# Kernel tuning notes

Measured on AMD Instinct MI355X. Metric: run time of the kernel, lower is better.

## Reference

```python
import jax, jax.numpy as jnp
import numpy as np

H = 16          # num_attention_heads
HD = 64         # attention_head_size
D = H * HD
SCALE = HD ** -0.5
SP_HEADS = np.array([0, 2, 4, 6, 8, 10, 12, 14])   # sparsemax heads
SM_HEADS = np.array([1, 3, 5, 7, 9, 11, 13, 15])   # softmax heads


def sparsemax(z):
    # z: [..., K]; sparsemax along last dim (Martins & Astudillo 2016)
    K = z.shape[-1]
    zs = -jnp.sort(-z, axis=-1)                      # descending sort
    k = jnp.arange(1, K + 1, dtype=z.dtype)
    cs = jnp.cumsum(zs, axis=-1)
    support = (1 + k * zs) > cs
    ksel = jnp.sum(support, axis=-1, keepdims=True)  # support size >= 1
    tau = (jnp.take_along_axis(cs, ksel - 1, axis=-1) - 1) / ksel.astype(z.dtype)
    return jnp.maximum(z - tau, 0)


def setup_inputs() -> dict:
    key = jax.random.key(0)
    ks = jax.random.split(key, 4)
    B, S = 4, 1024
    return {
        "hidden_states": jax.random.normal(ks[0], (B, S, D), dtype=jnp.float32),
        "Wq": jax.random.normal(ks[1], (D, D), dtype=jnp.float32) * 0.02,
        "bq": jnp.zeros((D,), dtype=jnp.float32),
        "Wk": jax.random.normal(ks[2], (D, D), dtype=jnp.float32) * 0.02,
        "bk": jnp.zeros((D,), dtype=jnp.float32),
        "Wv": jax.random.normal(ks[3], (D, D), dtype=jnp.float32) * 0.02,
        "bv": jnp.zeros((D,), dtype=jnp.float32),
        "attention_mask": jnp.zeros((B, 1, 1, S), dtype=jnp.float32),
    }


def reference(hidden_states, Wq, bq, Wk, bk, Wv, bv, attention_mask):
    B, S, _ = hidden_states.shape

    def proj(W, b):
        # [B,S,D] -> [B,H,S,HD]
        return (hidden_states @ W + b).reshape(B, S, H, HD).transpose(0, 2, 1, 3)

    q, k, v = proj(Wq, bq), proj(Wk, bk), proj(Wv, bv)
    scores = jnp.einsum('bhqd,bhkd->bhqk', q, k) * SCALE
    scores = scores + attention_mask
    scores = jnp.maximum(scores, -10000.0)           # clamp(min=-10000)
    weights = jnp.zeros_like(scores)
    weights = weights.at[:, SP_HEADS].set(sparsemax(scores[:, SP_HEADS]))
    weights = weights.at[:, SM_HEADS].set(jax.nn.softmax(scores[:, SM_HEADS], axis=-1))
    # dropout_p = 0 in eval mode
    attn_out = jnp.einsum('bhqk,bhkd->bhqd', weights, v)
    attn_out = attn_out.transpose(0, 2, 1, 3).reshape(B, S, D)
    return attn_out
```

## Files before the change

### kernel.cpp

```cpp
#include <hip/hip_runtime.h>
#include <hip/hip_bf16.h>
#include <stdint.h>

#define NH 16
#define HD 64
#define DM 1024
#define NB 4
#define SEQ 1024
#define NTOK (NB*SEQ)
#define SCALE 0.125f

typedef __bf16 bf16_t;
typedef __bf16 bf16x8 __attribute__((ext_vector_type(8)));
typedef __bf16 bf16x4 __attribute__((ext_vector_type(4)));
typedef float f32x4 __attribute__((ext_vector_type(4)));

typedef __attribute__((address_space(3))) unsigned char lds_byte;
typedef __attribute__((address_space(1))) const unsigned char gbl_byte;

__device__ __forceinline__ void glds16(const void* g, void* l){
  __builtin_amdgcn_global_load_lds((gbl_byte*)g, (lds_byte*)l, 16, 0, 0);
}

__global__ void cvt_hs_kernel(const float* __restrict__ in, bf16_t* __restrict__ out, int n4){
  int i = blockIdx.x*256 + threadIdx.x;
  if (i >= n4) return;
  f32x4 v = ((const f32x4*)in)[i];
  bf16x4 o;
  o[0]=(bf16_t)v[0]; o[1]=(bf16_t)v[1]; o[2]=(bf16_t)v[2]; o[3]=(bf16_t)v[3];
  ((bf16x4*)out)[i] = o;
}

__global__ void cvt_wt_kernel(const float* __restrict__ Wq, const float* __restrict__ Wk,
                              const float* __restrict__ Wv, bf16_t* __restrict__ outbase){
  __shared__ float tile[32][33];
  const float* W = blockIdx.z==0 ? Wq : (blockIdx.z==1 ? Wk : Wv);
  bf16_t* Wt = outbase + (size_t)blockIdx.z * DM * DM;
  int k0 = blockIdx.x*32, n0 = blockIdx.y*32;
  #pragma unroll
  for (int i=0;i<4;i++){
    int r = threadIdx.y + i*8;
    tile[r][threadIdx.x] = W[(size_t)(k0+r)*DM + n0 + threadIdx.x];
  }
  __syncthreads();
  #pragma unroll
  for (int i=0;i<4;i++){
    int r = threadIdx.y + i*8;
    Wt[(size_t)(n0+r)*DM + k0 + threadIdx.x] = (bf16_t)tile[threadIdx.x][r];
  }
}

__global__ __launch_bounds__(256)
void qkv_gemm_kernel(const bf16_t* __restrict__ Ag, const bf16_t* __restrict__ Wtb,
                     const float* __restrict__ bq, const float* __restrict__ bk, const float* __restrict__ bv,
                     bf16_t* __restrict__ Qb, bf16_t* __restrict__ Kb, bf16_t* __restrict__ Vtb)
{
  __shared__ __align__(16) bf16_t Asm[128*64];
  __shared__ __align__(16) bf16_t Bsm[128*64];
  const int z = blockIdx.z;
  const bf16_t* Btg = Wtb + (size_t)z*DM*DM;
  const float* bias = (z==0)?bq:((z==1)?bk:bv);
  const int m0 = blockIdx.x*128, n0 = blockIdx.y*128;
  const int tid = threadIdx.x, lane = tid&63, w = tid>>6;
  const int wr = w>>1, wc = w&1;
  const int lr = lane&15, hk = (lane>>4)<<3;

  f32x4 acc[4][4];
  #pragma unroll
  for (int a=0;a<4;a++)
    #pragma unroll
    for (int c=0;c<4;c++)
      acc[a][c] = (f32x4){0.f,0.f,0.f,0.f};

  for (int k0=0; k0<DM; k0+=64){
    #pragma unroll
    for (int i=0;i<4;i++){
      int cb = (i<<8) + (tid & 448);
      int flat = cb + lane;
      int row = flat>>3, kc = (flat&7)<<3;
      glds16(&Ag [(size_t)(m0+row)*DM + k0 + kc], &Asm[cb<<3]);
      glds16(&Btg[(size_t)(n0+row)*DM + k0 + kc], &Bsm[cb<<3]);
    }
    __syncthreads();
    #pragma unroll
    for (int kk=0;kk<2;kk++){
      bf16x8 af[4], bfv[4];
      #pragma unroll
      for (int mf=0;mf<4;mf++)
        af[mf] = *(const bf16x8*)&Asm[((wr*64 + mf*16 + lr)<<6) + (kk<<5) + hk];
      #pragma unroll
      for (int nf=0;nf<4;nf++)
        bfv[nf] = *(const bf16x8*)&Bsm[((wc*64 + nf*16 + lr)<<6) + (kk<<5) + hk];
      #pragma unroll
      for (int mf=0;mf<4;mf++)
        #pragma unroll
        for (int nf=0;nf<4;nf++)
          acc[mf][nf] = __builtin_amdgcn_mfma_f32_16x16x32_bf16(af[mf], bfv[nf], acc[mf][nf], 0, 0, 0);
    }
    __syncthreads();
  }

  const int q4 = (lane>>4)<<2;
  #pragma unroll
  for (int mf=0;mf<4;mf++){
    #pragma unroll
    for (int nf=0;nf<4;nf++){
      int gn = n0 + wc*64 + nf*16 + lr;
      float bsv = bias[gn];
      int hh = gn>>6, hd = gn&63;
      int gm0 = m0 + wr*64 + mf*16 + q4;
      int bb = gm0>>10, sq0 = gm0&1023;
      if (z < 2){
        bf16_t* dst = (z==0)?Qb:Kb;
        #pragma unroll
        for (int j=0;j<4;j++)
          dst[(((size_t)bb*NH + hh)*SEQ + (sq0+j))*HD + hd] = (bf16_t)(acc[mf][nf][j] + bsv);
      } else {
        bf16x4 pk;
        #pragma unroll
        for (int j=0;j<4;j++) pk[j] = (bf16_t)(acc[mf][nf][j] + bsv);
        *(bf16x4*)&Vtb[(((size_t)bb*NH + hh)*HD + hd)*SEQ + sq0] = pk;
      }
    }
  }
}

__device__ __forceinline__ void red4sum(float v[4]){
  #pragma unroll
  for (int m=32;m>=1;m>>=1){
    float t0=__shfl_xor(v[0],m,64), t1=__shfl_xor(v[1],m,64);
    float t2=__shfl_xor(v[2],m,64), t3=__shfl_xor(v[3],m,64);
    v[0]+=t0; v[1]+=t1; v[2]+=t2; v[3]+=t3;
  }
}
__device__ __forceinline__ void red4max(float v[4]){
  #pragma unroll
  for (int m=32;m>=1;m>>=1){
    float t0=__shfl_xor(v[0],m,64), t1=__shfl_xor(v[1],m,64);
    float t2=__shfl_xor(v[2],m,64), t3=__shfl_xor(v[3],m,64);
    v[0]=fmaxf(v[0],t0); v[1]=fmaxf(v[1],t1); v[2]=fmaxf(v[2],t2); v[3]=fmaxf(v[3],t3);
  }
}

__global__ __launch_bounds__(512, 4)
void attn_mfma2_kernel(const bf16_t* __restrict__ Qg, const bf16_t* __restrict__ Kg,
                       const bf16_t* __restrict__ Vt, const float* __restrict__ maskg,
                       float* __restrict__ outg)
{
  __shared__ __align__(16) bf16_t Sb[32*1024];
  char* Sbb = (char*)Sb;

  const int bh = blockIdx.y, b = bh>>4, h = bh&15;
  const int row0 = blockIdx.x*32;
  const int tid = threadIdx.x, lane = tid&63, w = tid>>6;
  const int ln = lane&15, hi4 = lane>>4;
  const size_t hoff = (size_t)bh*SEQ*HD;
  const int kbase = w*128;

  bf16x8 qf[2][2];
  #pragma unroll
  for (int mt=0; mt<2; ++mt)
    #pragma unroll
    for (int kt=0; kt<2; ++kt)
      qf[mt][kt] = *(const bf16x8*)&Qg[hoff + (size_t)(row0 + mt*16 + ln)*HD + kt*32 + hi4*8];

  #pragma unroll
  for (int nt=0; nt<8; ++nt){
    const int krow = kbase + nt*16;
    bf16x8 kf0 = *(const bf16x8*)&Kg[hoff + (size_t)(krow+ln)*HD +  0 + hi4*8];
    bf16x8 kf1 = *(const bf16x8*)&Kg[hoff + (size_t)(krow+ln)*HD + 32 + hi4*8];
    f32x4 mv = *(const f32x4*)&maskg[(size_t)b*SEQ + krow + hi4*4];
    #pragma unroll
    for (int mt=0; mt<2; ++mt){
      f32x4 acc = (f32x4){0.f,0.f,0.f,0.f};
      acc = __builtin_amdgcn_mfma_f32_16x16x32_bf16(kf0, qf[mt][0], acc, 0,0,0);
      acc = __builtin_amdgcn_mfma_f32_16x16x32_bf16(kf1, qf[mt][1], acc, 0,0,0);
      bf16x4 pk;
      #pragma unroll
      for (int j=0;j<4;++j)
        pk[j] = (bf16_t)fmaxf(fmaf(acc[j], SCALE, mv[j]), -10000.f);
      const int q = mt*16 + ln;
      const int g = (krow + hi4*4) >> 3;
      const int gp = g ^ ln;
      *(bf16x4*)(Sbb + q*2048 + gp*16 + (hi4&1)*8) = pk;
    }
  }
  __syncthreads();

  float z[4][16];
  const int qr = w*4;
  #pragma unroll
  for (int r=0;r<4;++r){
    const int q = qr + r;
    #pragma unroll
    for (int i=0;i<4;++i){
      const int gp = (i*32 + (lane>>1)) ^ (q&15);
      bf16x4 v4 = *(const bf16x4*)(Sbb + q*2048 + gp*16 + (lane&1)*8);
      z[r][i*4+0]=(float)v4[0]; z[r][i*4+1]=(float)v4[1];
      z[r][i*4+2]=(float)v4[2]; z[r][i*4+3]=(float)v4[3];
    }
  }
  __syncthreads();

  float mx[4];
  #pragma unroll
  for (int r=0;r<4;++r){
    float m = z[r][0];
    #pragma unroll
    for (int i=1;i<16;++i) m = fmaxf(m, z[r][i]);
    mx[r] = m;
  }
  red4max(mx);

  if ((h&1)==0){
    float lo[4], hi_[4];
    #pragma unroll
    for (int r=0;r<4;++r){ lo[r]=mx[r]-1.0f; hi_[r]=mx[r]; }
    for (int it=0; it<8; ++it){
      float mid[4], g4[4];
      #pragma unroll
      for (int r=0;r<4;++r){
        mid[r] = 0.5f*(lo[r]+hi_[r]);
        float g = 0.f;
        #pragma unroll
        for (int i=0;i<16;++i) g += fmaxf(z[r][i]-mid[r], 0.f);
        g4[r] = g;
      }
      red4sum(g4);
      #pragma unroll
      for (int r=0;r<4;++r){
        if (g4[r] >= 1.0f) lo[r] = mid[r]; else hi_[r] = mid[r];
      }
    }
    float tau[4];
    #pragma unroll
    for (int r=0;r<4;++r) tau[r] = lo[r];
    for (int it=0; it<3; ++it){
      float cnt[4], sm[4];
      #pragma unroll
      for (int r=0;r<4;++r){
        float c=0.f, s=0.f;
        #pragma unroll
        for (int i=0;i<16;++i){
          bool in = z[r][i] > tau[r];
          c += in ? 1.0f : 0.0f;
          s += in ? z[r][i] : 0.0f;
        }
        cnt[r]=c; sm[r]=s;
      }
      red4sum(cnt); red4sum(sm);
      #pragma unroll
      for (int r=0;r<4;++r) tau[r] = (sm[r]-1.0f)/cnt[r];
    }
    #pragma unroll
    for (int r=0;r<4;++r)
      #pragma unroll
      for (int i=0;i<16;++i) z[r][i] = fmaxf(z[r][i]-tau[r], 0.f);
  } else {
    float sm[4];
    #pragma unroll
    for (int r=0;r<4;++r){
      float s = 0.f;
      #pragma unroll
      for (int i=0;i<16;++i){ z[r][i] = __expf(z[r][i]-mx[r]); s += z[r][i]; }
      sm[r] = s;
    }
    red4sum(sm);
    #pragma unroll
    for (int r=0;r<4;++r){
      float inv = 1.0f/sm[r];
      #pragma unroll
      for (int i=0;i<16;++i) z[r][i] *= inv;
    }
  }

  #pragma unroll
  for (int r=0;r<4;++r){
    const int q = qr + r;
    #pragma unroll
    for (int i=0;i<4;++i){
      bf16x4 pk;
      pk[0]=(bf16_t)z[r][i*4+0]; pk[1]=(bf16_t)z[r][i*4+1];
      pk[2]=(bf16_t)z[r][i*4+2]; pk[3]=(bf16_t)z[r][i*4+3];
      const int gp = (i*32 + (lane>>1)) ^ (q&15);
      *(bf16x4*)(Sbb + q*2048 + gp*16 + (lane&1)*8) = pk;
    }
  }
  __syncthreads();

  const int mt = w>>2, hd0 = (w&3)*16;
  const bf16_t* vrow = Vt + (size_t)bh*HD*SEQ + (size_t)(hd0+ln)*SEQ;
  const char* wrow = Sbb + (mt*16+ln)*2048;
  f32x4 o0 = (f32x4){0.f,0.f,0.f,0.f}, o1 = (f32x4){0.f,0.f,0.f,0.f};
  #pragma unroll
  for (int kt=0; kt<32; kt+=2){
    bf16x8 wa0 = *(const bf16x8*)(wrow + ((((kt+0)*4+hi4) ^ ln)<<4));
    bf16x8 vb0 = *(const bf16x8*)&vrow[(kt+0)*32 + hi4*8];
    o0 = __builtin_amdgcn_mfma_f32_16x16x32_bf16(wa0, vb0, o0, 0,0,0);
    bf16x8 wa1 = *(const bf16x8*)(wrow + ((((kt+1)*4+hi4) ^ ln)<<4));
    bf16x8 vb1 = *(const bf16x8*)&vrow[(kt+1)*32 + hi4*8];
    o1 = __builtin_amdgcn_mfma_f32_16x16x32_bf16(wa1, vb1, o1, 0,0,0);
  }
  o0 += o1;
  #pragma unroll
  for (int j=0;j<4;++j)
    outg[(size_t)(b*SEQ + row0 + mt*16 + hi4*4 + j)*DM + h*64 + hd0 + ln] = o0[j];
}

extern "C" void kernel_launch(void* const* d_in, const int* in_sizes, int n_in,
                              void* d_out, int out_size, void* d_ws, size_t ws_size,
                              hipStream_t stream)
{
  const float* hs   = (const float*)d_in[0];
  const float* Wq   = (const float*)d_in[1];
  const float* bq   = (const float*)d_in[2];
  const float* Wk   = (const float*)d_in[3];
  const float* bk   = (const float*)d_in[4];
  const float* Wv   = (const float*)d_in[5];
  const float* bv   = (const float*)d_in[6];
  const float* mask = (const float*)d_in[7];
  float* out = (float*)d_out;

  char* ws = (char*)d_ws;
  bf16_t* hsb = (bf16_t*)ws;
  bf16_t* Wt  = (bf16_t*)(ws + (size_t)( 8u<<20));
  bf16_t* Qb  = (bf16_t*)(ws + (size_t)(14u<<20));
  bf16_t* Kb  = (bf16_t*)(ws + (size_t)(22u<<20));
  bf16_t* Vtb = (bf16_t*)(ws + (size_t)(30u<<20));

  cvt_hs_kernel<<<(NTOK*DM/4 + 255)/256, 256, 0, stream>>>(hs, hsb, NTOK*DM/4);
  cvt_wt_kernel<<<dim3(32,32,3), dim3(32,8), 0, stream>>>(Wq, Wk, Wv, Wt);
  qkv_gemm_kernel<<<dim3(32,8,3), 256, 0, stream>>>(hsb, Wt, bq, bk, bv, Qb, Kb, Vtb);
  attn_mfma2_kernel<<<dim3(32,64), 512, 0, stream>>>(Qb, Kb, Vtb, mask, out);
}
```

Baseline: 317.0 us.

## Coalesce QKV and attention epilogues via LDS, add V transpose, XCD-aware grid

The QKV GEMM epilogue now stages the biased bf16 tile in shared memory and writes full 128-byte rows to Q/K/V in head-major layout, replacing scattered 2-byte stores. V is written untransposed, and a new kernel transposes it into the reused hidden-state buffer. The attention kernel stages its output through LDS for coalesced float4 stores and uses a flat grid that places blocks of the same head on the same XCD to improve L2 reuse of K/V. This adds an extra kernel launch and a round-trip of V through memory.

```diff
diff --git a/kernel.cpp b/kernel.cpp
--- a/kernel.cpp
+++ b/kernel.cpp
@@ -53,13 +53,16 @@
 __global__ __launch_bounds__(256)
 void qkv_gemm_kernel(const bf16_t* __restrict__ Ag, const bf16_t* __restrict__ Wtb,
                      const float* __restrict__ bq, const float* __restrict__ bk, const float* __restrict__ bv,
-                     bf16_t* __restrict__ Qb, bf16_t* __restrict__ Kb, bf16_t* __restrict__ Vtb)
+                     bf16_t* __restrict__ Qb, bf16_t* __restrict__ Kb, bf16_t* __restrict__ Vb)
 {
-  __shared__ __align__(16) bf16_t Asm[128*64];
-  __shared__ __align__(16) bf16_t Bsm[128*64];
+  __shared__ __align__(16) bf16_t smem[2*128*64];
+  bf16_t* Asm = smem;
+  bf16_t* Bsm = smem + 128*64;
+  bf16_t* Csm = smem;
   const int z = blockIdx.z;
   const bf16_t* Btg = Wtb + (size_t)z*DM*DM;
   const float* bias = (z==0)?bq:((z==1)?bk:bv);
+  bf16_t* dst = (z==0)?Qb:((z==1)?Kb:Vb);
   const int m0 = blockIdx.x*128, n0 = blockIdx.y*128;
   const int tid = threadIdx.x, lane = tid&63, w = tid>>6;
   const int wr = w>>1, wc = w&1;
@@ -105,24 +108,49 @@
   for (int mf=0;mf<4;mf++){
     #pragma unroll
     for (int nf=0;nf<4;nf++){
-      int gn = n0 + wc*64 + nf*16 + lr;
-      float bsv = bias[gn];
-      int hh = gn>>6, hd = gn&63;
-      int gm0 = m0 + wr*64 + mf*16 + q4;
-      int bb = gm0>>10, sq0 = gm0&1023;
-      if (z < 2){
-        bf16_t* dst = (z==0)?Qb:Kb;
-        #pragma unroll
-        for (int j=0;j<4;j++)
-          dst[(((size_t)bb*NH + hh)*SEQ + (sq0+j))*HD + hd] = (bf16_t)(acc[mf][nf][j] + bsv);
-      } else {
-        bf16x4 pk;
-        #pragma unroll
-        for (int j=0;j<4;j++) pk[j] = (bf16_t)(acc[mf][nf][j] + bsv);
-        *(bf16x4*)&Vtb[(((size_t)bb*NH + hh)*HD + hd)*SEQ + sq0] = pk;
-      }
-    }
-  }
+      int col = wc*64 + nf*16 + lr;
+      float bsv = bias[n0 + col];
+      #pragma unroll
+      for (int j=0;j<4;j++)
+        Csm[(wr*64 + mf*16 + q4 + j)*128 + col] = (bf16_t)(acc[mf][nf][j] + bsv);
+    }
+  }
+  __syncthreads();
+  {
+    int row = tid>>1, half = tid&1;
+    int gm = m0 + row, bb = gm>>10, sq = gm&1023;
+    int hh = (n0 + half*64)>>6;
+    const bf16x8* src = (const bf16x8*)&Csm[row*128 + half*64];
+    bf16x8* d = (bf16x8*)&dst[(((size_t)bb*NH + hh)*SEQ + sq)*HD];
+    #pragma unroll
+    for (int c=0;c<8;c++) d[c] = src[c];
+  }
+}
+
+__global__ __launch_bounds__(256)
+void v_tr_kernel(const bf16_t* __restrict__ Vb, bf16_t* __restrict__ Vt){
+  __shared__ __align__(16) bf16_t T[64*64];
+  const int bh = blockIdx.y, sq0 = blockIdx.x*64;
+  const int t = threadIdx.x;
+  const bf16_t* src = Vb + ((size_t)bh*SEQ + sq0)*HD;
+  #pragma unroll
+  for (int i=0;i<2;i++){
+    int flat = i*256 + t;
+    int r = flat>>3, ch = flat&7;
+    bf16x8 v = *(const bf16x8*)&src[r*HD + ch*8];
+    *(bf16x8*)((char*)T + r*128 + ((ch ^ (r&7))*16)) = v;
+  }
+  __syncthreads();
+  const int hd = t>>2, part = t&3;
+  bf16_t tmp[16];
+  #pragma unroll
+  for (int s=0;s<16;s++){
+    int sq = part*16 + s;
+    tmp[s] = *(const bf16_t*)((char*)T + sq*128 + (((hd>>3) ^ (sq&7))*16) + (hd&7)*2);
+  }
+  bf16_t* d = Vt + ((size_t)bh*HD + hd)*SEQ + sq0 + part*16;
+  *(bf16x8*)&d[0] = *(const bf16x8*)&tmp[0];
+  *(bf16x8*)&d[8] = *(const bf16x8*)&tmp[8];
 }
 
 __device__ __forceinline__ void red4sum(float v[4]){
@@ -150,8 +178,11 @@
   __shared__ __align__(16) bf16_t Sb[32*1024];
   char* Sbb = (char*)Sb;
 
-  const int bh = blockIdx.y, b = bh>>4, h = bh&15;
-  const int row0 = blockIdx.x*32;
+  const int flat = blockIdx.x;
+  const int xcd = flat & 7, jj = flat >> 3;
+  const int bh = ((jj>>5)<<3) | xcd;
+  const int row0 = (jj&31)*32;
+  const int b = bh>>4, h = bh&15;
   const int tid = threadIdx.x, lane = tid&63, w = tid>>6;
   const int ln = lane&15, hi4 = lane>>4;
   const size_t hoff = (size_t)bh*SEQ*HD;
@@ -302,9 +333,17 @@
     o1 = __builtin_amdgcn_mfma_f32_16x16x32_bf16(wa1, vb1, o1, 0,0,0);
   }
   o0 += o1;
+
+  __syncthreads();
+  float* Ob = (float*)Sbb;
   #pragma unroll
   for (int j=0;j<4;++j)
-    outg[(size_t)(b*SEQ + row0 + mt*16 + hi4*4 + j)*DM + h*64 + hd0 + ln] = o0[j];
+    Ob[(mt*16 + hi4*4 + j)*64 + hd0 + ln] = o0[j];
+  __syncthreads();
+  {
+    int rr = tid>>4, c4 = (tid&15)<<2;
+    *(f32x4*)&outg[(size_t)(b*SEQ + row0 + rr)*DM + h*64 + c4] = *(const f32x4*)&Ob[rr*64 + c4];
+  }
 }
 
 extern "C" void kernel_launch(void* const* d_in, const int* in_sizes, int n_in,
@@ -326,10 +365,12 @@
   bf16_t* Wt  = (bf16_t*)(ws + (size_t)( 8u<<20));
   bf16_t* Qb  = (bf16_t*)(ws + (size_t)(14u<<20));
   bf16_t* Kb  = (bf16_t*)(ws + (size_t)(22u<<20));
-  bf16_t* Vtb = (bf16_t*)(ws + (size_t)(30u<<20));
+  bf16_t* Vb  = (bf16_t*)(ws + (size_t)(30u<<20));
+  bf16_t* Vt  = hsb;
 
   cvt_hs_kernel<<<(NTOK*DM/4 + 255)/256, 256, 0, stream>>>(hs, hsb, NTOK*DM/4);
   cvt_wt_kernel<<<dim3(32,32,3), dim3(32,8), 0, stream>>>(Wq, Wk, Wv, Wt);
-  qkv_gemm_kernel<<<dim3(32,8,3), 256, 0, stream>>>(hsb, Wt, bq, bk, bv, Qb, Kb, Vtb);
-  attn_mfma2_kernel<<<dim3(32,64), 512, 0, stream>>>(Qb, Kb, Vtb, mask, out);
-}
+  qkv_gemm_kernel<<<dim3(32,8,3), 256, 0, stream>>>(hsb, Wt, bq, bk, bv, Qb, Kb, Vb);
+  v_tr_kernel<<<dim3(16,64), 256, 0, stream>>>(Vb, Vt);
+  attn_mfma2_kernel<<<2048, 512, 0, stream>>>(Qb, Kb, Vt, mask, out);
+}
```

New measurement: 320.2 us. Within noise of the previous version (+1.0%).
